# Kernel tuning notes

Measured on AMD Instinct MI355X. Metric: run time of the kernel, lower is better.

The kernel has to match this reference:

```python
import jax, jax.numpy as jnp
import numpy as np

MAX_CAV = 5


def setup_inputs() -> dict:
    key = jax.random.key(0)
    k1, k2, k3, k4, k5 = jax.random.split(key, 5)
    # ragged group lengths, each <= MAX_CAV, sum = 25
    record_len = jnp.array([3, 5, 2, 4, 1, 5, 3, 2], dtype=jnp.int32)
    N, C, H, W = 25, 256, 48, 176
    x = jax.random.normal(k1, (N, C, H, W), dtype=jnp.float32)
    W1 = jax.random.normal(k2, (MAX_CAV, 2 * MAX_CAV), dtype=jnp.float32) * 0.3
    W2 = jax.random.normal(k3, (MAX_CAV, MAX_CAV), dtype=jnp.float32) * 0.3
    conv_w = jax.random.normal(k4, (MAX_CAV,), dtype=jnp.float32) * 0.3
    conv_b = jax.random.normal(k5, (1,), dtype=jnp.float32) * 0.1
    return dict(x=x, record_len=record_len, W1=W1, W2=W2, conv_w=conv_w, conv_b=conv_b)


def _pad_regroup(x, record_len, max_cav):
    # scatter ragged tokens into a zero-padded [bs, max_cav, C, H, W] buffer
    N = x.shape[0]
    bs = record_len.shape[0]
    cum = jnp.cumsum(record_len)
    tok = jnp.arange(N)
    b = jnp.searchsorted(cum, tok, side='right')      # batch id per token
    slot = tok - (cum[b] - record_len[b])             # position within group
    padded = jnp.zeros((bs, max_cav) + x.shape[1:], x.dtype)
    return padded.at[b, slot].set(x)


def reference(x, record_len, W1, W2, conv_w, conv_b):
    padded = _pad_regroup(x, record_len, MAX_CAV)     # [bs, M, C, H, W]
    # AdaptiveAvg/MaxPool3d(1) over (C,H,W); padded slots are all-zero -> max=0
    x_avg = padded.mean(axis=(2, 3, 4))               # [bs, M]
    x_max = padded.max(axis=(2, 3, 4))                # [bs, M]
    x_sq = jnp.concatenate([x_avg, x_max], axis=1)    # [bs, 2M]
    gate = jax.nn.relu(jax.nn.sigmoid(x_sq @ W1.T) @ W2.T)  # [bs, M]
    scaled = padded * gate[:, :, None, None, None]
    # 1x1x1 Conv3d(M -> 1) == weighted sum over CAV axis + bias, then ReLU
    out = jax.nn.relu(jnp.einsum('m,bmchw->bchw', conv_w, scaled) + conv_b[0])
    return out
```

## Files before the change

kernel.cpp:

```cpp
#include <hip/hip_runtime.h>
#include <hip/hip_bf16.h>
#include <math.h>

#define CHW      2162688
#define V4       540672
#define BPT      64
#define V4_BLK   8448
#define ITERS    33
#define MAXCAV   5

__global__ __launch_bounds__(256) void k_reduce(const float4* __restrict__ x,
                                                float* __restrict__ psum,
                                                float* __restrict__ pmax) {
    const int t   = blockIdx.y;
    const int blk = blockIdx.x;
    const long base = (long)t * V4 + (long)blk * V4_BLK;

    float s = 0.0f;
    float mx = -INFINITY;
    #pragma unroll 4
    for (int i = 0; i < ITERS; ++i) {
        float4 v = x[base + i * 256 + threadIdx.x];
        s += (v.x + v.y) + (v.z + v.w);
        mx = fmaxf(mx, fmaxf(fmaxf(v.x, v.y), fmaxf(v.z, v.w)));
    }

    __shared__ float ssum[256];
    __shared__ float smax[256];
    ssum[threadIdx.x] = s;
    smax[threadIdx.x] = mx;
    __syncthreads();
    #pragma unroll
    for (int off = 128; off > 0; off >>= 1) {
        if (threadIdx.x < off) {
            ssum[threadIdx.x] += ssum[threadIdx.x + off];
            smax[threadIdx.x] = fmaxf(smax[threadIdx.x], smax[threadIdx.x + off]);
        }
        __syncthreads();
    }
    if (threadIdx.x == 0) {
        psum[t * BPT + blk] = ssum[0];
        pmax[t * BPT + blk] = smax[0];
    }
}

__global__ __launch_bounds__(256) void k_gate(const float* __restrict__ psum,
                                              const float* __restrict__ pmax,
                                              const int*   __restrict__ record_len,
                                              const float* __restrict__ W1,
                                              const float* __restrict__ W2,
                                              const float* __restrict__ conv_w,
                                              int*   __restrict__ starts,
                                              float* __restrict__ coefs,
                                              int bs, int ntok) {
    __shared__ float tsum[32];
    __shared__ float tmax[32];
    const int wave = threadIdx.x >> 6;
    const int lane = threadIdx.x & 63;

    for (int t = wave; t < ntok; t += 4) {
        float s = psum[t * BPT + lane];
        float m = pmax[t * BPT + lane];
        #pragma unroll
        for (int off = 32; off > 0; off >>= 1) {
            s += __shfl_xor(s, off, 64);
            m = fmaxf(m, __shfl_xor(m, off, 64));
        }
        if (lane == 0) { tsum[t] = s; tmax[t] = m; }
    }
    __syncthreads();

    if ((int)threadIdx.x < bs) {
        const int b = threadIdx.x;
        int start = 0;
        for (int i = 0; i < b; ++i) start += record_len[i];
        const int len = record_len[b];

        float xsq[2 * MAXCAV];
        #pragma unroll
        for (int m = 0; m < MAXCAV; ++m) {
            const bool valid = m < len;
            xsq[m]          = valid ? tsum[start + m] * (1.0f / (float)CHW) : 0.0f;
            xsq[MAXCAV + m] = valid ? tmax[start + m] : 0.0f;
        }
        float h[MAXCAV];
        #pragma unroll
        for (int j = 0; j < MAXCAV; ++j) {
            float a = 0.0f;
            #pragma unroll
            for (int k = 0; k < 2 * MAXCAV; ++k) a += xsq[k] * W1[j * 2 * MAXCAV + k];
            h[j] = 1.0f / (1.0f + expf(-a));
        }
        starts[b] = start;
        #pragma unroll
        for (int m = 0; m < MAXCAV; ++m) {
            float g = 0.0f;
            #pragma unroll
            for (int j = 0; j < MAXCAV; ++j) g += h[j] * W2[m * MAXCAV + j];
            g = fmaxf(g, 0.0f);
            coefs[b * MAXCAV + m] = conv_w[m] * g;
        }
    }
}

template <int LEN>
__device__ __forceinline__ void apply_body(const float4* __restrict__ x,
                                           const float* __restrict__ c,
                                           float bias, int start,
                                           long obase, int idx,
                                           float4* __restrict__ out) {
    float4 acc = make_float4(bias, bias, bias, bias);
    #pragma unroll
    for (int m = 0; m < LEN; ++m) {
        float4 v = x[(long)(start + m) * V4 + idx];
        acc.x += c[m] * v.x;
        acc.y += c[m] * v.y;
        acc.z += c[m] * v.z;
        acc.w += c[m] * v.w;
    }
    acc.x = fmaxf(acc.x, 0.0f);
    acc.y = fmaxf(acc.y, 0.0f);
    acc.z = fmaxf(acc.z, 0.0f);
    acc.w = fmaxf(acc.w, 0.0f);
    out[obase + idx] = acc;
}

__global__ __launch_bounds__(256) void k_apply(const float4* __restrict__ x,
                                               const int*   __restrict__ record_len,
                                               const int*   __restrict__ starts,
                                               const float* __restrict__ coefs,
                                               const float* __restrict__ conv_b,
                                               float4* __restrict__ out) {
    const int b     = blockIdx.y;
    const int len   = record_len[b];
    const int start = starts[b];
    float c[MAXCAV];
    #pragma unroll
    for (int m = 0; m < MAXCAV; ++m) c[m] = coefs[b * MAXCAV + m];
    const float bias  = conv_b[0];
    const long  obase = (long)b * V4;

    int idx = blockIdx.x * 1024 + threadIdx.x;
    #pragma unroll
    for (int r = 0; r < 4; ++r, idx += 256) {
        switch (len) {
            case 1: apply_body<1>(x, c, bias, start, obase, idx, out); break;
            case 2: apply_body<2>(x, c, bias, start, obase, idx, out); break;
            case 3: apply_body<3>(x, c, bias, start, obase, idx, out); break;
            case 4: apply_body<4>(x, c, bias, start, obase, idx, out); break;
            default: apply_body<5>(x, c, bias, start, obase, idx, out); break;
        }
    }
}

extern "C" void kernel_launch(void* const* d_in, const int* in_sizes, int n_in,
                              void* d_out, int out_size, void* d_ws, size_t ws_size,
                              hipStream_t stream) {
    const float* x  = (const float*)d_in[0];
    const int*   rl = (const int*)d_in[1];
    const float* W1 = (const float*)d_in[2];
    const float* W2 = (const float*)d_in[3];
    const float* cw = (const float*)d_in[4];
    const float* cb = (const float*)d_in[5];
    float4* out = (float4*)d_out;

    char* ws = (char*)d_ws;
    float* psum   = (float*)(ws);
    float* pmax   = (float*)(ws + 6400);
    int*   starts = (int*)  (ws + 12800);
    float* coefs  = (float*)(ws + 12832);

    const int ntok = in_sizes[0] / CHW;
    const int bs   = in_sizes[1];

    k_reduce<<<dim3(BPT, ntok), 256, 0, stream>>>((const float4*)x, psum, pmax);
    k_gate<<<1, 256, 0, stream>>>(psum, pmax, rl, W1, W2, cw, starts, coefs, bs, ntok);
    k_apply<<<dim3(V4 / 1024, bs), 256, 0, stream>>>((const float4*)x, rl, starts, coefs, cb, out);
}
```

Measured before the change: 88.63 us.

## Loop over batches inside apply kernel and use nontemporal output stores

The apply kernel now launches a 1D grid over spatial chunks, with each block processing two float4 elements per thread and looping over all batch groups itself, instead of using a 2D grid with one batch per blockIdx.y. Output writes use nontemporal stores so the write-once output does not pollute cache. The aim is to reduce block count and cache pressure from streaming output; the risk is less parallelism per block and a serialized loop over batches lengthening each block.

```diff
diff --git a/kernel.cpp b/kernel.cpp
--- a/kernel.cpp
+++ b/kernel.cpp
@@ -8,6 +8,8 @@
 #define V4_BLK   8448
 #define ITERS    33
 #define MAXCAV   5
+
+typedef float f32x4 __attribute__((ext_vector_type(4)));
 
 __global__ __launch_bounds__(256) void k_reduce(const float4* __restrict__ x,
                                                 float* __restrict__ psum,
@@ -104,25 +106,36 @@
 }
 
 template <int LEN>
-__device__ __forceinline__ void apply_body(const float4* __restrict__ x,
-                                           const float* __restrict__ c,
-                                           float bias, int start,
-                                           long obase, int idx,
-                                           float4* __restrict__ out) {
-    float4 acc = make_float4(bias, bias, bias, bias);
+__device__ __forceinline__ void apply_one(const float4* __restrict__ x,
+                                          const float* __restrict__ c,
+                                          float bias, int start,
+                                          long obase, int idx,
+                                          float4* __restrict__ out) {
+    float ax = bias, ay = bias, az = bias, aw = bias;
     #pragma unroll
     for (int m = 0; m < LEN; ++m) {
         float4 v = x[(long)(start + m) * V4 + idx];
-        acc.x += c[m] * v.x;
-        acc.y += c[m] * v.y;
-        acc.z += c[m] * v.z;
-        acc.w += c[m] * v.w;
+        ax += c[m] * v.x;
+        ay += c[m] * v.y;
+        az += c[m] * v.z;
+        aw += c[m] * v.w;
     }
-    acc.x = fmaxf(acc.x, 0.0f);
-    acc.y = fmaxf(acc.y, 0.0f);
-    acc.z = fmaxf(acc.z, 0.0f);
-    acc.w = fmaxf(acc.w, 0.0f);
-    out[obase + idx] = acc;
+    f32x4 acc;
+    acc.x = fmaxf(ax, 0.0f);
+    acc.y = fmaxf(ay, 0.0f);
+    acc.z = fmaxf(az, 0.0f);
+    acc.w = fmaxf(aw, 0.0f);
+    __builtin_nontemporal_store(acc, (f32x4*)(out + obase + idx));
+}
+
+template <int LEN>
+__device__ __forceinline__ void apply_pair(const float4* __restrict__ x,
+                                           const float* __restrict__ c,
+                                           float bias, int start,
+                                           long obase, int idx0,
+                                           float4* __restrict__ out) {
+    apply_one<LEN>(x, c, bias, start, obase, idx0, out);
+    apply_one<LEN>(x, c, bias, start, obase, idx0 + 256, out);
 }
 
 __global__ __launch_bounds__(256) void k_apply(const float4* __restrict__ x,
@@ -130,25 +143,25 @@
                                                const int*   __restrict__ starts,
                                                const float* __restrict__ coefs,
                                                const float* __restrict__ conv_b,
-                                               float4* __restrict__ out) {
-    const int b     = blockIdx.y;
-    const int len   = record_len[b];
-    const int start = starts[b];
-    float c[MAXCAV];
-    #pragma unroll
-    for (int m = 0; m < MAXCAV; ++m) c[m] = coefs[b * MAXCAV + m];
-    const float bias  = conv_b[0];
-    const long  obase = (long)b * V4;
+                                               float4* __restrict__ out,
+                                               int bs) {
+    const int idx0 = blockIdx.x * 512 + threadIdx.x;
+    const float bias = conv_b[0];
 
-    int idx = blockIdx.x * 1024 + threadIdx.x;
-    #pragma unroll
-    for (int r = 0; r < 4; ++r, idx += 256) {
+    for (int b = 0; b < bs; ++b) {
+        const int len   = record_len[b];
+        const int start = starts[b];
+        float c[MAXCAV];
+        #pragma unroll
+        for (int m = 0; m < MAXCAV; ++m) c[m] = coefs[b * MAXCAV + m];
+        const long obase = (long)b * V4;
+
         switch (len) {
-            case 1: apply_body<1>(x, c, bias, start, obase, idx, out); break;
-            case 2: apply_body<2>(x, c, bias, start, obase, idx, out); break;
-            case 3: apply_body<3>(x, c, bias, start, obase, idx, out); break;
-            case 4: apply_body<4>(x, c, bias, start, obase, idx, out); break;
-            default: apply_body<5>(x, c, bias, start, obase, idx, out); break;
+            case 1:  apply_pair<1>(x, c, bias, start, obase, idx0, out); break;
+            case 2:  apply_pair<2>(x, c, bias, start, obase, idx0, out); break;
+            case 3:  apply_pair<3>(x, c, bias, start, obase, idx0, out); break;
+            case 4:  apply_pair<4>(x, c, bias, start, obase, idx0, out); break;
+            default: apply_pair<5>(x, c, bias, start, obase, idx0, out); break;
         }
     }
 }
@@ -175,5 +188,5 @@
 
     k_reduce<<<dim3(BPT, ntok), 256, 0, stream>>>((const float4*)x, psum, pmax);
     k_gate<<<1, 256, 0, stream>>>(psum, pmax, rl, W1, W2, cw, starts, coefs, bs, ntok);
-    k_apply<<<dim3(V4 / 1024, bs), 256, 0, stream>>>((const float4*)x, rl, starts, coefs, cb, out);
+    k_apply<<<V4 / 512, 256, 0, stream>>>((const float4*)x, rl, starts, coefs, cb, out, bs);
 }
```

After: 84.66 us. 4.5% less time.
